# Kernel tuning notes

Measured on AMD Instinct MI355X. Metric: run time of the kernel, lower is better.

The kernel has to match this reference:

```python
import jax, jax.numpy as jnp
import numpy as np

B, N, F_IN, T = 4, 512, 64, 16
K, F_CHEB, F_TIME, TS = 3, 64, 64, 1
E = 16384
LN_EPS = 1e-5


def setup_inputs() -> dict:
    key = jax.random.key(0)
    ks = jax.random.split(key, 18)
    s = 0.05
    X = jax.random.normal(ks[0], (B, N, F_IN, T), jnp.float32)
    # edges with guaranteed no self-loops (so remove_self_loops is a no-op)
    src = jax.random.randint(ks[1], (E,), 0, N, jnp.int32)
    off = jax.random.randint(ks[2], (E,), 1, N, jnp.int32)
    dst = (src + off) % N
    edge_index = jnp.stack([src, dst])
    return {
        'X': X,
        'edge_index': edge_index,
        'U1': jax.random.uniform(ks[3], (N,)) * s,
        'U2': jax.random.normal(ks[4], (F_IN, N)) * s,
        'U3': jax.random.uniform(ks[5], (F_IN,)) * s,
        'be': jax.random.normal(ks[6], (1, T, T)) * s,
        'Ve': jax.random.normal(ks[7], (T, T)) * s,
        'Ws1': jax.random.uniform(ks[8], (T,)) * s,
        'Ws2': jax.random.normal(ks[9], (F_IN, T)) * s,
        'Ws3': jax.random.uniform(ks[10], (F_IN,)) * s,
        'bs': jax.random.normal(ks[11], (1, N, N)) * s,
        'Vs': jax.random.normal(ks[12], (N, N)) * s,
        'W_cheb': jax.random.normal(ks[13], (K, F_IN, F_CHEB)) * s,
        'b_cheb': jax.random.uniform(ks[14], (F_CHEB,)) * s,
        'Wt': jax.random.normal(ks[15], (F_TIME, F_CHEB, 1, 3)) * s,
        'bt': jnp.zeros((F_TIME,), jnp.float32),
        'Wr': jax.random.normal(ks[16], (F_TIME, F_IN, 1, 1)) * s,
        'br': jnp.zeros((F_TIME,), jnp.float32),
        'gamma': jnp.ones((F_TIME,), jnp.float32),
        'beta': jnp.zeros((F_TIME,), jnp.float32),
    }


def _forward(edge_index, X, U1, U2, U3, be, Ve, Ws1, Ws2, Ws3, bs, Vs,
             W_cheb, b_cheb, Wt, bt, Wr, br, gamma, beta):
    Bn, Nn, Fn, Tn = X.shape
    # ---- temporal attention: (B,T,T)
    lhs_t = jnp.einsum('bnft,n->btf', X, U1) @ U2            # (B,T,N)
    rhs_t = jnp.einsum('f,bnft->bnt', U3, X)                 # (B,N,T)
    Et = jnp.matmul(Ve, jax.nn.sigmoid(jnp.matmul(lhs_t, rhs_t) + be))
    Et = jax.nn.softmax(Et, axis=1)
    # temporally re-weighted signal
    Xt = jnp.matmul(X.reshape(Bn, Nn * Fn, Tn), Et).reshape(Bn, Nn, Fn, Tn)
    # ---- spatial attention: (B,N,N)
    lhs_s = jnp.einsum('bnft,t->bnf', Xt, Ws1) @ Ws2         # (B,N,T)
    rhs_s = jnp.einsum('f,bnft->btn', Ws3, Xt)               # (B,T,N)
    S = jnp.matmul(Vs, jax.nn.sigmoid(jnp.matmul(lhs_s, rhs_s) + bs))
    S = jax.nn.softmax(S, axis=1)                            # (B,N,N)
    # ---- scaled sym-normalized Laplacian; lambda_max=2 so 2/lambda_max = 1.
    # edges: -D^-1/2 A D^-1/2 (E), +I self loops (N), then add_self_loops(-1) (N)
    row, col = edge_index[0], edge_index[1]
    ew = jnp.ones(row.shape, X.dtype)
    deg = jnp.zeros((Nn,), X.dtype).at[row].add(ew)
    dis = jnp.where(deg > 0, 1.0 / jnp.sqrt(jnp.maximum(deg, 1.0)), 0.0)  # deg is integral so max() only guards deg==0
    wn = -dis[row] * dis[col]
    loops = jnp.arange(Nn)
    rows = jnp.concatenate([row, loops, loops])
    cols = jnp.concatenate([col, loops, loops])
    norm = jnp.concatenate([wn, jnp.ones((Nn,), X.dtype), -jnp.ones((Nn,), X.dtype)])
    att_norm = norm[None, :] * S[:, rows, cols]              # (B,Etot)

    def prop(h, w):
        # propagate over transposed edges: gather at col, scatter-add at row
        # h: (B,T,N,F); w broadcastable to (B,1,Etot)
        msg = w[..., None] * h[:, :, cols, :]
        return jnp.zeros_like(h).at[:, :, rows, :].add(msg)

    xt = X.transpose(0, 3, 1, 2)                             # (B,T,N,F): ChebConv applied per timestep
    Tx0 = jnp.diagonal(S, axis1=1, axis2=2)[:, None, :, None] * xt  # diag(S) @ x
    out = jnp.einsum('btnf,fg->btng', Tx0, W_cheb[0])
    if W_cheb.shape[0] > 1:
        Tx1 = prop(Tx0, att_norm[:, None, :])
        out = out + jnp.einsum('btnf,fg->btng', Tx1, W_cheb[1])
    for k in range(2, W_cheb.shape[0]):
        Tx2 = 2.0 * prop(Tx1, norm[None, None, :]) - Tx0
        out = out + jnp.einsum('btnf,fg->btng', Tx2, W_cheb[k])
        Tx0, Tx1 = Tx1, Tx2
    X_hat = jax.nn.relu(out + b_cheb)                        # (B,T,N,Fc)
    # ---- time conv (1x3, stride (1,TS)) on (B,Fc,N,T) + residual 1x1 conv
    conv_t = jax.lax.conv_general_dilated(
        X_hat.transpose(0, 3, 2, 1), Wt, (1, TS), ((0, 0), (1, 1)),
        dimension_numbers=('NCHW', 'OIHW', 'NCHW')) + bt[None, :, None, None]
    conv_r = jax.lax.conv_general_dilated(
        X.transpose(0, 2, 1, 3), Wr, (1, TS), ((0, 0), (0, 0)),
        dimension_numbers=('NCHW', 'OIHW', 'NCHW')) + br[None, :, None, None]
    Z = jax.nn.relu(conv_r + conv_t).transpose(0, 3, 2, 1)   # (B,T,N,Ft)
    mu = jnp.mean(Z, -1, keepdims=True)
    var = jnp.var(Z, -1, keepdims=True)
    Z = (Z - mu) / jnp.sqrt(var + LN_EPS) * gamma + beta     # LayerNorm over Ft
    return Z.transpose(0, 2, 3, 1)                           # (B,N,Ft,T)


def reference(X, edge_index, U1, U2, U3, be, Ve, Ws1, Ws2, Ws3, bs, Vs,
              W_cheb, b_cheb, Wt, bt, Wr, br, gamma, beta):
    return _forward(edge_index, X, U1, U2, U3, be, Ve, Ws1, Ws2, Ws3, bs, Vs,
                    W_cheb, b_cheb, Wt, bt, Wr, br, gamma, beta)
```

## Files before the change

### kernel.cpp

```cpp
#include <hip/hip_runtime.h>
#include <math.h>

#define NB 4
#define NV 512
#define NF 64
#define NT 16
#define NE 16384

#define TX1_OFF    2097152u
#define SIGT_OFF   4194304u
#define ST_OFF     TX1_OFF
#define BST_OFF    8388608u
#define ET_OFF     8650752u
#define PART_OFF   8651776u
#define RHST_OFF   8684544u
#define LHSS_OFF   8717312u
#define RHSSN_OFF  8750080u
#define DIAGS_OFF  8782848u
#define CSRW_OFF   8850432u
#define WTT_OFF    8866816u
#define WRT_OFF    8879104u
#define RHS3_OFF   8883712u
#define EW1_OFF    8916480u
#define MPART_OFF  8916544u
#define FEND       8949312u

__global__ void k_prep(const int* __restrict__ ei, int* __restrict__ counts,
                       const float* __restrict__ Wt, const float* __restrict__ Wr,
                       const float* __restrict__ bs,
                       float* __restrict__ WtT, float* __restrict__ WrT,
                       float* __restrict__ bsT,
                       const float* __restrict__ X, const float* __restrict__ U1,
                       const float* __restrict__ U3, const float* __restrict__ Ws3,
                       float* __restrict__ part, float* __restrict__ rhs,
                       float* __restrict__ rhs3) {
    __shared__ int h[512];
    __shared__ float tile[64][65];
    int bid = blockIdx.x, tid = threadIdx.x;
    if (bid < 64) {
        int c = bid;
        h[tid] = 0; h[tid + 256] = 0;
        __syncthreads();
        atomicAdd(&h[ei[c * 256 + tid]], 1);
        __syncthreads();
        counts[c * 512 + tid] = h[tid];
        counts[c * 512 + tid + 256] = h[tid + 256];
    } else if (bid < 128) {
        int tb = bid - 64;
        int r0 = (tb >> 3) * 64, c0 = (tb & 7) * 64;
        int c = tid & 63, rq = tid >> 6;
        for (int k = 0; k < 16; ++k) {
            int r = rq * 16 + k;
            tile[r][c] = bs[(r0 + r) * 512 + c0 + c];
        }
        __syncthreads();
        int r2 = tid & 63;
        for (int k = 0; k < 16; ++k) {
            int c2 = rq * 16 + k;
            bsT[(size_t)(c0 + c2) * 512 + r0 + r2] = tile[r2][c2];
        }
    } else if (bid < 192) {
        int idx = (bid - 128) * 256 + tid;
        if (idx < 12288) {
            int o = idx & 63, gd = idx >> 6;
            int g = gd / 3, dt = gd - g * 3;
            WtT[idx] = Wt[(o * 64 + g) * 3 + dt];
        } else {
            int i2 = idx - 12288;
            int o = i2 & 63, f = i2 >> 6;
            WrT[i2] = Wr[o * 64 + f];
        }
    } else {
        int sub = bid - 192;
        if (sub < 32) {
            int b = sub >> 3, g = sub & 7;
            float acc[4] = {0.f, 0.f, 0.f, 0.f};
            const float* Xb = X + (size_t)b * NV * 1024;
            int n0 = g * 64;
            for (int nn = 0; nn < 64; ++nn) {
                int n = n0 + nn;
                float u = U1[n];
                const float* xp = Xb + (size_t)n * 1024;
#pragma unroll
                for (int k = 0; k < 4; ++k) acc[k] += xp[tid + 256 * k] * u;
            }
#pragma unroll
            for (int k = 0; k < 4; ++k) part[(size_t)(b * 8 + g) * 1024 + tid + 256 * k] = acc[k];
        } else {
            int gid = (sub - 32) * 256 + tid;
            int t = gid & 15;
            const float* xp = X + ((size_t)(gid >> 4)) * 1024 + t;
            float a = 0.f, a3 = 0.f;
#pragma unroll
            for (int f = 0; f < 64; ++f) {
                float v = xp[f * 16];
                a += U3[f] * v;
                a3 += Ws3[f] * v;
            }
            rhs[gid] = a;
            rhs3[gid] = a3;
        }
    }
}

__global__ __launch_bounds__(512) void k_graph(const int* __restrict__ ei,
                                               const int* __restrict__ counts,
                                               int* __restrict__ row_start,
                                               int* __restrict__ csr_col,
                                               float* __restrict__ csr_w,
                                               const float* __restrict__ rhs_g,
                                               const float* __restrict__ U2,
                                               float* __restrict__ Mpart) {
    __shared__ int sc[512];
    __shared__ int base_l[512];
    __shared__ float dis_l[512];
    __shared__ int rs_l[512];
    __shared__ int rowL[256];
    __shared__ float rhsL[1024];
    int bid = blockIdx.x, tid = threadIdx.x;
    if (bid < 64) {
        int c = bid;
        int r = tid;
        int sum = 0, base = 0;
        for (int cc = 0; cc < 64; ++cc) {
            if (cc == c) base = sum;
            sum += counts[cc * 512 + r];
        }
        base_l[r] = base;
        dis_l[r] = sum > 0 ? 1.0f / sqrtf((float)sum) : 0.0f;
        sc[r] = sum;
        __syncthreads();
        for (int off = 1; off < 512; off <<= 1) {
            int v = sc[r];
            int add = (r >= off) ? sc[r - off] : 0;
            __syncthreads();
            sc[r] = v + add;
            __syncthreads();
        }
        rs_l[r] = sc[r] - sum;
        if (c == 0) {
            row_start[r] = sc[r] - sum;
            if (r == 511) row_start[512] = sc[r];
        }
        if (tid < 256) rowL[tid] = ei[c * 256 + tid];
        __syncthreads();
        if (tid < 256) {
            int rr = rowL[tid];
            int col = ei[NE + c * 256 + tid];
            int rank = 0;
            for (int j = 0; j < tid; ++j)
                if (rowL[j] == rr) rank++;
            int pos = rs_l[rr] + base_l[rr] + rank;
            csr_col[pos] = col;
            csr_w[pos] = -dis_l[rr] * dis_l[col];
        }
    } else {
        int sub = bid - 64;
        int b = sub >> 3, g = sub & 7;
        rhsL[tid] = rhs_g[(size_t)b * 8192 + g * 1024 + tid];
        rhsL[tid + 512] = rhs_g[(size_t)b * 8192 + g * 1024 + tid + 512];
        __syncthreads();
        float acc[2] = {0.f, 0.f};
        int fA[2], tA[2];
#pragma unroll
        for (int k = 0; k < 2; ++k) { int idx = tid + 512 * k; fA[k] = idx >> 4; tA[k] = idx & 15; }
        int n0 = g * 64;
        for (int nn = 0; nn < 64; ++nn) {
#pragma unroll
            for (int k = 0; k < 2; ++k)
                acc[k] += U2[fA[k] * 512 + n0 + nn] * rhsL[nn * 16 + tA[k]];
        }
#pragma unroll
        for (int k = 0; k < 2; ++k) Mpart[(size_t)(b * 8 + g) * 1024 + tid + 512 * k] = acc[k];
    }
}

__global__ void k_temporal(const float* __restrict__ part, const float* __restrict__ Mpart,
                           const float* __restrict__ be,
                           const float* __restrict__ Ve, const float* __restrict__ Ws1,
                           float* __restrict__ Et, float* __restrict__ ew1) {
    __shared__ float lhs1[1024];
    __shared__ float M[1024];
    __shared__ float Esig[256];
    __shared__ float Et0[256];
    __shared__ float red[32];
    __shared__ float EtL[256];
    int b = blockIdx.x, tid = threadIdx.x;
#pragma unroll
    for (int k = 0; k < 4; ++k) {
        int idx = tid + 256 * k;
        float s = 0.f, m = 0.f;
        for (int g = 0; g < 8; ++g) {
            s += part[(size_t)(b * 8 + g) * 1024 + idx];
            m += Mpart[(size_t)(b * 8 + g) * 1024 + idx];
        }
        lhs1[idx] = s;
        M[idx] = m;
    }
    __syncthreads();
    {
        int t1 = tid >> 4, t2 = tid & 15;
        float s = 0.f;
        for (int f = 0; f < 64; ++f) s += lhs1[f * 16 + t1] * M[f * 16 + t2];
        s += be[t1 * 16 + t2];
        Esig[tid] = 1.f / (1.f + expf(-s));
    }
    __syncthreads();
    {
        int t1 = tid >> 4, t2 = tid & 15;
        float s = 0.f;
        for (int k = 0; k < 16; ++k) s += Ve[t1 * 16 + k] * Esig[k * 16 + t2];
        Et0[tid] = s;
    }
    __syncthreads();
    if (tid < 16) {
        float m = -1e30f;
        for (int k = 0; k < 16; ++k) m = fmaxf(m, Et0[k * 16 + tid]);
        float s = 0.f;
        for (int k = 0; k < 16; ++k) s += expf(Et0[k * 16 + tid] - m);
        red[tid] = m; red[16 + tid] = 1.f / s;
    }
    __syncthreads();
    {
        int t2 = tid & 15;
        float etv = expf(Et0[tid] - red[t2]) * red[16 + t2];
        Et[b * 256 + tid] = etv;
        EtL[tid] = etv;
    }
    __syncthreads();
    if (tid < 16) {
        float s = 0.f;
        for (int t = 0; t < 16; ++t) s += EtL[tid * 16 + t] * Ws1[t];
        ew1[b * 16 + tid] = s;
    }
}

__global__ __launch_bounds__(256) void k_spat2(const float* __restrict__ X,
                                               const float* __restrict__ ew1,
                                               const float* __restrict__ rhs3,
                                               const float* __restrict__ Et,
                                               const float* __restrict__ Ws2,
                                               float* __restrict__ lhs_s,
                                               float* __restrict__ rhs_sn) {
    int wv = threadIdx.x >> 6, lane = threadIdx.x & 63;
    int bn = blockIdx.x * 4 + wv;
    int b = bn >> 9;
    const float4* xp = (const float4*)(X + (size_t)bn * 1024 + lane * 16);
    float4 x0 = xp[0], x1 = xp[1], x2 = xp[2], x3 = xp[3];
    const float* e1 = ew1 + b * 16;
    float l1 = x0.x * e1[0] + x0.y * e1[1] + x0.z * e1[2] + x0.w * e1[3]
             + x1.x * e1[4] + x1.y * e1[5] + x1.z * e1[6] + x1.w * e1[7]
             + x2.x * e1[8] + x2.y * e1[9] + x2.z * e1[10] + x2.w * e1[11]
             + x3.x * e1[12] + x3.y * e1[13] + x3.z * e1[14] + x3.w * e1[15];
    const float4* wp = (const float4*)(Ws2 + lane * 16);
    float4 w0 = wp[0], w1 = wp[1], w2 = wp[2], w3 = wp[3];
    float p[16] = {l1 * w0.x, l1 * w0.y, l1 * w0.z, l1 * w0.w,
                   l1 * w1.x, l1 * w1.y, l1 * w1.z, l1 * w1.w,
                   l1 * w2.x, l1 * w2.y, l1 * w2.z, l1 * w2.w,
                   l1 * w3.x, l1 * w3.y, l1 * w3.z, l1 * w3.w};
#pragma unroll
    for (int off = 32; off; off >>= 1) {
#pragma unroll
        for (int k = 0; k < 16; ++k) p[k] += __shfl_xor(p[k], off);
    }
    if (lane == 0) {
        float4* lp = (float4*)(lhs_s + (size_t)bn * 16);
        lp[0] = make_float4(p[0], p[1], p[2], p[3]);
        lp[1] = make_float4(p[4], p[5], p[6], p[7]);
        lp[2] = make_float4(p[8], p[9], p[10], p[11]);
        lp[3] = make_float4(p[12], p[13], p[14], p[15]);
    }
    if (lane < 16) {
        const float* r3 = rhs3 + (size_t)bn * 16;
        const float* Eb = Et + b * 256;
        float s = 0.f;
#pragma unroll
        for (int tp = 0; tp < 16; ++tp) s += r3[tp] * Eb[tp * 16 + lane];
        rhs_sn[(size_t)bn * 16 + lane] = s;
    }
}

__global__ void k_sigT(const float* __restrict__ lhs_s, const float* __restrict__ rhs_sn,
                       const float* __restrict__ bsT, float* __restrict__ sigT) {
    int gid = blockIdx.x * 256 + threadIdx.x;
    int k = gid & 511, j = (gid >> 9) & 511, b = gid >> 18;
    const float4* lp = (const float4*)(lhs_s + (size_t)(b * 512 + k) * 16);
    const float4* rp = (const float4*)(rhs_sn + (size_t)(b * 512 + j) * 16);
    float s = 0.f;
#pragma unroll
    for (int q = 0; q < 4; ++q) {
        float4 a = lp[q], c = rp[q];
        s += a.x * c.x + a.y * c.y + a.z * c.z + a.w * c.w;
    }
    s += bsT[(size_t)j * 512 + k];
    sigT[gid] = 1.f / (1.f + expf(-s));
}

__global__ __launch_bounds__(256) void k_gemm_s(const float* __restrict__ sigT,
                                                const float* __restrict__ Vs,
                                                float* __restrict__ S0T) {
    __shared__ float As[32 * 68];
    __shared__ float Bs[32 * 68];
    int bI = blockIdx.x, bJ = blockIdx.y, b = blockIdx.z;
    int tid = threadIdx.x, tx = tid & 15, ty = tid >> 4;
    float acc[4][4] = {};
    const float* Ab = sigT + ((size_t)b * 512 + bJ * 64) * 512;
    const float* Bb = Vs + (size_t)bI * 64 * 512;
    for (int k0 = 0; k0 < 512; k0 += 32) {
#pragma unroll
        for (int p = 0; p < 2; ++p) {
            int idx = tid + 256 * p;
            int row = idx >> 3, kk = (idx & 7) * 4;
            float4 a = *(const float4*)(Ab + (size_t)row * 512 + k0 + kk);
            As[(kk + 0) * 68 + row] = a.x; As[(kk + 1) * 68 + row] = a.y;
            As[(kk + 2) * 68 + row] = a.z; As[(kk + 3) * 68 + row] = a.w;
            float4 v = *(const float4*)(Bb + (size_t)row * 512 + k0 + kk);
            Bs[(kk + 0) * 68 + row] = v.x; Bs[(kk + 1) * 68 + row] = v.y;
            Bs[(kk + 2) * 68 + row] = v.z; Bs[(kk + 3) * 68 + row] = v.w;
        }
        __syncthreads();
#pragma unroll
        for (int kk = 0; kk < 32; ++kk) {
            float4 a = *(const float4*)(As + kk * 68 + ty * 4);
            float4 bv = *(const float4*)(Bs + kk * 68 + tx * 4);
            acc[0][0] += a.x * bv.x; acc[0][1] += a.x * bv.y; acc[0][2] += a.x * bv.z; acc[0][3] += a.x * bv.w;
            acc[1][0] += a.y * bv.x; acc[1][1] += a.y * bv.y; acc[1][2] += a.y * bv.z; acc[1][3] += a.y * bv.w;
            acc[2][0] += a.z * bv.x; acc[2][1] += a.z * bv.y; acc[2][2] += a.z * bv.z; acc[2][3] += a.z * bv.w;
            acc[3][0] += a.w * bv.x; acc[3][1] += a.w * bv.y; acc[3][2] += a.w * bv.z; acc[3][3] += a.w * bv.w;
        }
        __syncthreads();
    }
    float* Cb = S0T + ((size_t)b * 512 + bJ * 64) * 512 + bI * 64;
#pragma unroll
    for (int y = 0; y < 4; ++y) {
        int j = ty * 4 + y;
        *(float4*)(Cb + (size_t)j * 512 + tx * 4) =
            make_float4(acc[y][0], acc[y][1], acc[y][2], acc[y][3]);
    }
}

__global__ void k_softmax_s(float* __restrict__ ST, float* __restrict__ diagS) {
    __shared__ float red[4];
    int bj = blockIdx.x;
    int b = bj >> 9, j = bj & 511;
    float* row = ST + (size_t)bj * 512;
    int tid = threadIdx.x;
    float v0 = row[tid], v1 = row[tid + 256];
    float m = fmaxf(v0, v1);
    for (int off = 32; off; off >>= 1) m = fmaxf(m, __shfl_xor(m, off));
    if ((tid & 63) == 0) red[tid >> 6] = m;
    __syncthreads();
    m = fmaxf(fmaxf(red[0], red[1]), fmaxf(red[2], red[3]));
    __syncthreads();
    float e0 = expf(v0 - m), e1 = expf(v1 - m);
    float s = e0 + e1;
    for (int off = 32; off; off >>= 1) s += __shfl_xor(s, off);
    if ((tid & 63) == 0) red[tid >> 6] = s;
    __syncthreads();
    s = red[0] + red[1] + red[2] + red[3];
    float inv = 1.f / s;
    float r0 = e0 * inv, r1 = e1 * inv;
    row[tid] = r0;
    row[tid + 256] = r1;
    if (j < 256) { if (tid == j) diagS[b * 512 + j] = r0; }
    else { if (tid == j - 256) diagS[b * 512 + j] = r1; }
}

__global__ __launch_bounds__(256) void k_prop1(const float* __restrict__ X,
                                               const float* __restrict__ ST,
                                               const float* __restrict__ diagS,
                                               const float* __restrict__ csr_w,
                                               const int* __restrict__ csr_col,
                                               const int* __restrict__ row_start,
                                               float* __restrict__ Tx1) {
    int blk = ((blockIdx.x & 7) << 8) + (blockIdx.x >> 3);
    int b = blk >> 9, i = blk & 511;
    int tid = threadIdx.x;
    int s = row_start[i], e2 = row_start[i + 1];
    const float4* Xb = (const float4*)(X + (size_t)b * 512 * 1024);
    const float* STb = ST + (size_t)b * 512 * 512;
    const float* dSb = diagS + b * 512;
    float4 acc = make_float4(0.f, 0.f, 0.f, 0.f);
    for (int p = s; p < e2; ++p) {
        int col = csr_col[p];
        float w = csr_w[p] * STb[(size_t)col * 512 + i] * dSb[col];
        float4 v = Xb[col * 256 + tid];
        acc.x += w * v.x; acc.y += w * v.y; acc.z += w * v.z; acc.w += w * v.w;
    }
    *(float4*)(Tx1 + (size_t)blk * 1024 + tid * 4) = acc;
}

__global__ __launch_bounds__(256) void k_pco(const float* __restrict__ X,
                                             const float* __restrict__ Tx1,
                                             const float* __restrict__ diagS,
                                             const float* __restrict__ csr_w,
                                             const int* __restrict__ csr_col,
                                             const int* __restrict__ row_start,
                                             const float* __restrict__ Wc,
                                             const float* __restrict__ bc,
                                             const float* __restrict__ WtT,
                                             const float* __restrict__ WrT,
                                             const float* __restrict__ bt,
                                             const float* __restrict__ br,
                                             const float* __restrict__ gamma,
                                             const float* __restrict__ beta,
                                             float* __restrict__ out) {
    __shared__ float buf[4160];
    __shared__ float xl[1024];
    __shared__ float xh[1280];
    int blk = ((blockIdx.x & 7) << 8) + (blockIdx.x >> 3);
    int b = blk >> 9, i = blk & 511;
    int tid = threadIdx.x;
#pragma unroll
    for (int k = 0; k < 5; ++k) xh[tid + 256 * k] = 0.f;
    int s = row_start[i], e2 = row_start[i + 1];
    const float* T1b = Tx1 + (size_t)b * 512 * 1024 + tid * 4;
    float4 acc = make_float4(0.f, 0.f, 0.f, 0.f);
    for (int p = s; p < e2; ++p) {
        int col = csr_col[p];
        float w = csr_w[p];
        float4 v = *(const float4*)(T1b + (size_t)col * 1024);
        acc.x += w * v.x; acc.y += w * v.y; acc.z += w * v.z; acc.w += w * v.w;
    }
    float ds = diagS[blk];
    size_t roff = (size_t)blk * 1024 + tid * 4;
    float4 x0 = *(const float4*)(X + roff);
    float4 t1v = *(const float4*)(Tx1 + roff);
    float4 t0v, t2v;
    t2v.x = 2.f * acc.x - ds * x0.x;
    t2v.y = 2.f * acc.y - ds * x0.y;
    t2v.z = 2.f * acc.z - ds * x0.z;
    t2v.w = 2.f * acc.w - ds * x0.w;
    t0v.x = x0.x * ds; t0v.y = x0.y * ds; t0v.z = x0.z * ds; t0v.w = x0.w * ds;
    *(float4*)(buf + tid * 4) = t0v;
    *(float4*)(buf + 1024 + tid * 4) = t1v;
    *(float4*)(buf + 2048 + tid * 4) = t2v;
    *(float4*)(xl + tid * 4) = x0;
    __syncthreads();
    {
        int g = tid >> 2, t4 = (tid & 3) * 4;
        float bcg = bc[g];
        float4 accg = make_float4(bcg, bcg, bcg, bcg);
        const float* t0s = buf;
        const float* t1s = buf + 1024;
        const float* t2s = buf + 2048;
        for (int f = 0; f < 64; ++f) {
            float w0 = Wc[f * 64 + g];
            float w1 = Wc[4096 + f * 64 + g];
            float w2 = Wc[8192 + f * 64 + g];
            float4 a0 = *(const float4*)(t0s + f * 16 + t4);
            float4 a1 = *(const float4*)(t1s + f * 16 + t4);
            float4 a2 = *(const float4*)(t2s + f * 16 + t4);
            accg.x += w0 * a0.x + w1 * a1.x + w2 * a2.x;
            accg.y += w0 * a0.y + w1 * a1.y + w2 * a2.y;
            accg.z += w0 * a0.z + w1 * a1.z + w2 * a2.z;
            accg.w += w0 * a0.w + w1 * a1.w + w2 * a2.w;
        }
        xh[g * 20 + t4 + 1] = fmaxf(accg.x, 0.f);
        xh[g * 20 + t4 + 2] = fmaxf(accg.y, 0.f);
        xh[g * 20 + t4 + 3] = fmaxf(accg.z, 0.f);
        xh[g * 20 + t4 + 4] = fmaxf(accg.w, 0.f);
    }
    __syncthreads();
    float* red = buf;
    int o = tid & 63, q = tid >> 6;
    float accv[16];
#pragma unroll
    for (int k = 0; k < 16; ++k) accv[k] = 0.f;
    for (int gi = 0; gi < 16; ++gi) {
        int g = q * 16 + gi;
        const float4* xp = (const float4*)(xh + g * 20);
        float4 xa = xp[0], xb = xp[1], xc = xp[2], xd = xp[3], xe = xp[4];
        float xs[20] = {xa.x, xa.y, xa.z, xa.w, xb.x, xb.y, xb.z, xb.w,
                        xc.x, xc.y, xc.z, xc.w, xd.x, xd.y, xd.z, xd.w,
                        xe.x, xe.y, xe.z, xe.w};
        float w0 = WtT[(g * 3 + 0) * 64 + o];
        float w1 = WtT[(g * 3 + 1) * 64 + o];
        float w2 = WtT[(g * 3 + 2) * 64 + o];
#pragma unroll
        for (int tt = 0; tt < 16; ++tt)
            accv[tt] += xs[tt] * w0 + xs[tt + 1] * w1 + xs[tt + 2] * w2;
    }
    for (int fi = 0; fi < 16; ++fi) {
        int f = q * 16 + fi;
        const float4* xp = (const float4*)(xl + f * 16);
        float4 xa = xp[0], xb = xp[1], xc = xp[2], xd = xp[3];
        float xs[16] = {xa.x, xa.y, xa.z, xa.w, xb.x, xb.y, xb.z, xb.w,
                        xc.x, xc.y, xc.z, xc.w, xd.x, xd.y, xd.z, xd.w};
        float w = WrT[f * 64 + o];
#pragma unroll
        for (int tt = 0; tt < 16; ++tt) accv[tt] += xs[tt] * w;
    }
#pragma unroll
    for (int tt = 0; tt < 16; ++tt) red[q * 1024 + tt * 64 + o] = accv[tt];
    __syncthreads();
    float bsum = bt[o] + br[o];
    float go = gamma[o], bo = beta[o];
    float zv4[4];
#pragma unroll
    for (int tt = 0; tt < 4; ++tt) {
        int t = q * 4 + tt;
        float sv = bsum;
#pragma unroll
        for (int qq = 0; qq < 4; ++qq) sv += red[qq * 1024 + t * 64 + o];
        zv4[tt] = fmaxf(sv, 0.f);
    }
    __syncthreads();
#pragma unroll
    for (int tt = 0; tt < 4; ++tt) {
        int t = q * 4 + tt;
        float zv = zv4[tt];
        float sv = zv, sq = zv * zv;
        for (int off = 32; off; off >>= 1) {
            sv += __shfl_xor(sv, off);
            sq += __shfl_xor(sq, off);
        }
        float mu = sv * (1.f / 64.f);
        float var = sq * (1.f / 64.f) - mu * mu;
        red[t * 65 + o] = (zv - mu) * rsqrtf(var + 1e-5f) * go + bo;
    }
    __syncthreads();
#pragma unroll
    for (int k = 0; k < 4; ++k) {
        int idx = tid + 256 * k;
        out[(size_t)blk * 1024 + idx] = red[(idx & 15) * 65 + (idx >> 4)];
    }
}

extern "C" void kernel_launch(void* const* d_in, const int* in_sizes, int n_in,
                              void* d_out, int out_size, void* d_ws, size_t ws_size,
                              hipStream_t stream) {
    const float* X     = (const float*)d_in[0];
    const int*   ei    = (const int*)d_in[1];
    const float* U1    = (const float*)d_in[2];
    const float* U2    = (const float*)d_in[3];
    const float* U3    = (const float*)d_in[4];
    const float* be    = (const float*)d_in[5];
    const float* Ve    = (const float*)d_in[6];
    const float* Ws1   = (const float*)d_in[7];
    const float* Ws2   = (const float*)d_in[8];
    const float* Ws3   = (const float*)d_in[9];
    const float* bs    = (const float*)d_in[10];
    const float* Vs    = (const float*)d_in[11];
    const float* Wc    = (const float*)d_in[12];
    const float* bc    = (const float*)d_in[13];
    const float* Wt    = (const float*)d_in[14];
    const float* bt    = (const float*)d_in[15];
    const float* Wr    = (const float*)d_in[16];
    const float* br    = (const float*)d_in[17];
    const float* gamma = (const float*)d_in[18];
    const float* beta  = (const float*)d_in[19];

    float* ws = (float*)d_ws;
    float* Tx1    = ws + TX1_OFF;
    float* ST     = ws + ST_OFF;
    float* sigT   = ws + SIGT_OFF;
    float* bsT    = ws + BST_OFF;
    float* Et     = ws + ET_OFF;
    float* part   = ws + PART_OFF;
    float* rhs_t  = ws + RHST_OFF;
    float* lhs_s  = ws + LHSS_OFF;
    float* rhs_sn = ws + RHSSN_OFF;
    float* diagS  = ws + DIAGS_OFF;
    float* csr_w  = ws + CSRW_OFF;
    float* WtT    = ws + WTT_OFF;
    float* WrT    = ws + WRT_OFF;
    float* rhs3   = ws + RHS3_OFF;
    float* ew1    = ws + EW1_OFF;
    float* Mpart  = ws + MPART_OFF;

    int* ib        = (int*)(ws + FEND);
    int* row_start = ib;
    int* csr_col   = ib + 516;
    int* counts    = csr_col + NE;

    k_prep<<<352, 256, 0, stream>>>(ei, counts, Wt, Wr, bs, WtT, WrT, bsT,
                                    X, U1, U3, Ws3, part, rhs_t, rhs3);
    k_graph<<<96, 512, 0, stream>>>(ei, counts, row_start, csr_col, csr_w,
                                    rhs_t, U2, Mpart);

    k_temporal<<<4, 256, 0, stream>>>(part, Mpart, be, Ve, Ws1, Et, ew1);

    k_spat2<<<512, 256, 0, stream>>>(X, ew1, rhs3, Et, Ws2, lhs_s, rhs_sn);
    k_sigT<<<4096, 256, 0, stream>>>(lhs_s, rhs_sn, bsT, sigT);
    k_gemm_s<<<dim3(8, 8, 4), 256, 0, stream>>>(sigT, Vs, ST);
    k_softmax_s<<<2048, 256, 0, stream>>>(ST, diagS);

    k_prop1<<<2048, 256, 0, stream>>>(X, ST, diagS, csr_w, csr_col, row_start, Tx1);
    k_pco<<<2048, 256, 0, stream>>>(X, Tx1, diagS, csr_w, csr_col, row_start,
                                    Wc, bc, WtT, WrT, bt, br, gamma, beta,
                                    (float*)d_out);
}
```

Baseline: 146.7 us.

## Transpose Cheb weights, fold T0 scaling, and split time-conv work by time groups

Adds a transposed copy of the Chebyshev weights in the prep kernel so each thread in k_pco reads its weights as contiguous float4. The T0 term is now formed on the fly from the shared X tile times diagS, which drops one shared buffer. The time conv and residual conv are restructured so each thread computes all 64 input channels for 4 time steps, instead of 16 time steps over a quarter of the channels. This removes the cross-quarter shared-memory reduction and one barrier, at the cost of longer per-thread loops with more weight loads.

```diff
diff --git a/kernel.cpp b/kernel.cpp
--- a/kernel.cpp
+++ b/kernel.cpp
@@ -23,13 +23,14 @@
 #define RHS3_OFF   8883712u
 #define EW1_OFF    8916480u
 #define MPART_OFF  8916544u
-#define FEND       8949312u
+#define WCT_OFF    8949312u
+#define FEND       8961600u
 
 __global__ void k_prep(const int* __restrict__ ei, int* __restrict__ counts,
                        const float* __restrict__ Wt, const float* __restrict__ Wr,
-                       const float* __restrict__ bs,
+                       const float* __restrict__ Wc, const float* __restrict__ bs,
                        float* __restrict__ WtT, float* __restrict__ WrT,
-                       float* __restrict__ bsT,
+                       float* __restrict__ WcT, float* __restrict__ bsT,
                        const float* __restrict__ X, const float* __restrict__ U1,
                        const float* __restrict__ U3, const float* __restrict__ Ws3,
                        float* __restrict__ part, float* __restrict__ rhs,
@@ -70,8 +71,13 @@
             int o = i2 & 63, f = i2 >> 6;
             WrT[i2] = Wr[o * 64 + f];
         }
+    } else if (bid < 240) {
+        int idx = (bid - 192) * 256 + tid;
+        int g = idx / 192, rem = idx - g * 192;
+        int k = rem >> 6, f = rem & 63;
+        WcT[idx] = Wc[k * 4096 + f * 64 + g];
     } else {
-        int sub = bid - 192;
+        int sub = bid - 240;
         if (sub < 32) {
             int b = sub >> 3, g = sub & 7;
             float acc[4] = {0.f, 0.f, 0.f, 0.f};
@@ -396,7 +402,7 @@
                                              const float* __restrict__ csr_w,
                                              const int* __restrict__ csr_col,
                                              const int* __restrict__ row_start,
-                                             const float* __restrict__ Wc,
+                                             const float* __restrict__ WcT,
                                              const float* __restrict__ bc,
                                              const float* __restrict__ WtT,
                                              const float* __restrict__ WrT,
@@ -405,7 +411,7 @@
                                              const float* __restrict__ gamma,
                                              const float* __restrict__ beta,
                                              float* __restrict__ out) {
-    __shared__ float buf[4160];
+    __shared__ float buf[2048];
     __shared__ float xl[1024];
     __shared__ float xh[1280];
     int blk = ((blockIdx.x & 7) << 8) + (blockIdx.x >> 3);
@@ -426,35 +432,41 @@
     size_t roff = (size_t)blk * 1024 + tid * 4;
     float4 x0 = *(const float4*)(X + roff);
     float4 t1v = *(const float4*)(Tx1 + roff);
-    float4 t0v, t2v;
+    float4 t2v;
     t2v.x = 2.f * acc.x - ds * x0.x;
     t2v.y = 2.f * acc.y - ds * x0.y;
     t2v.z = 2.f * acc.z - ds * x0.z;
     t2v.w = 2.f * acc.w - ds * x0.w;
-    t0v.x = x0.x * ds; t0v.y = x0.y * ds; t0v.z = x0.z * ds; t0v.w = x0.w * ds;
-    *(float4*)(buf + tid * 4) = t0v;
-    *(float4*)(buf + 1024 + tid * 4) = t1v;
-    *(float4*)(buf + 2048 + tid * 4) = t2v;
+    *(float4*)(buf + tid * 4) = t1v;
+    *(float4*)(buf + 1024 + tid * 4) = t2v;
     *(float4*)(xl + tid * 4) = x0;
     __syncthreads();
     {
         int g = tid >> 2, t4 = (tid & 3) * 4;
         float bcg = bc[g];
         float4 accg = make_float4(bcg, bcg, bcg, bcg);
-        const float* t0s = buf;
-        const float* t1s = buf + 1024;
-        const float* t2s = buf + 2048;
-        for (int f = 0; f < 64; ++f) {
-            float w0 = Wc[f * 64 + g];
-            float w1 = Wc[4096 + f * 64 + g];
-            float w2 = Wc[8192 + f * 64 + g];
-            float4 a0 = *(const float4*)(t0s + f * 16 + t4);
-            float4 a1 = *(const float4*)(t1s + f * 16 + t4);
-            float4 a2 = *(const float4*)(t2s + f * 16 + t4);
-            accg.x += w0 * a0.x + w1 * a1.x + w2 * a2.x;
-            accg.y += w0 * a0.y + w1 * a1.y + w2 * a2.y;
-            accg.z += w0 * a0.z + w1 * a1.z + w2 * a2.z;
-            accg.w += w0 * a0.w + w1 * a1.w + w2 * a2.w;
+        const float* t1s = buf;
+        const float* t2s = buf + 1024;
+        const float* wgp = WcT + g * 192;
+        for (int f0 = 0; f0 < 64; f0 += 4) {
+            float4 wq0 = *(const float4*)(wgp + f0);
+            float4 wq1 = *(const float4*)(wgp + 64 + f0);
+            float4 wq2 = *(const float4*)(wgp + 128 + f0);
+#pragma unroll
+            for (int ff = 0; ff < 4; ++ff) {
+                int f = f0 + ff;
+                float w0 = ff == 0 ? wq0.x : ff == 1 ? wq0.y : ff == 2 ? wq0.z : wq0.w;
+                float w1 = ff == 0 ? wq1.x : ff == 1 ? wq1.y : ff == 2 ? wq1.z : wq1.w;
+                float w2 = ff == 0 ? wq2.x : ff == 1 ? wq2.y : ff == 2 ? wq2.z : wq2.w;
+                float4 xv = *(const float4*)(xl + f * 16 + t4);
+                float4 a1 = *(const float4*)(t1s + f * 16 + t4);
+                float4 a2 = *(const float4*)(t2s + f * 16 + t4);
+                float a0x = ds * xv.x, a0y = ds * xv.y, a0z = ds * xv.z, a0w = ds * xv.w;
+                accg.x += w0 * a0x + w1 * a1.x + w2 * a2.x;
+                accg.y += w0 * a0y + w1 * a1.y + w2 * a2.y;
+                accg.z += w0 * a0z + w1 * a1.z + w2 * a2.z;
+                accg.w += w0 * a0w + w1 * a1.w + w2 * a2.w;
+            }
         }
         xh[g * 20 + t4 + 1] = fmaxf(accg.x, 0.f);
         xh[g * 20 + t4 + 2] = fmaxf(accg.y, 0.f);
@@ -462,54 +474,30 @@
         xh[g * 20 + t4 + 4] = fmaxf(accg.w, 0.f);
     }
     __syncthreads();
-    float* red = buf;
-    int o = tid & 63, q = tid >> 6;
-    float accv[16];
-#pragma unroll
-    for (int k = 0; k < 16; ++k) accv[k] = 0.f;
-    for (int gi = 0; gi < 16; ++gi) {
-        int g = q * 16 + gi;
-        const float4* xp = (const float4*)(xh + g * 20);
-        float4 xa = xp[0], xb = xp[1], xc = xp[2], xd = xp[3], xe = xp[4];
-        float xs[20] = {xa.x, xa.y, xa.z, xa.w, xb.x, xb.y, xb.z, xb.w,
-                        xc.x, xc.y, xc.z, xc.w, xd.x, xd.y, xd.z, xd.w,
-                        xe.x, xe.y, xe.z, xe.w};
+    float* z = buf;
+    int o = tid & 63, tg = tid >> 6;
+    float accv[4] = {0.f, 0.f, 0.f, 0.f};
+    for (int g = 0; g < 64; ++g) {
         float w0 = WtT[(g * 3 + 0) * 64 + o];
         float w1 = WtT[(g * 3 + 1) * 64 + o];
         float w2 = WtT[(g * 3 + 2) * 64 + o];
-#pragma unroll
-        for (int tt = 0; tt < 16; ++tt)
-            accv[tt] += xs[tt] * w0 + xs[tt + 1] * w1 + xs[tt + 2] * w2;
-    }
-    for (int fi = 0; fi < 16; ++fi) {
-        int f = q * 16 + fi;
-        const float4* xp = (const float4*)(xl + f * 16);
-        float4 xa = xp[0], xb = xp[1], xc = xp[2], xd = xp[3];
-        float xs[16] = {xa.x, xa.y, xa.z, xa.w, xb.x, xb.y, xb.z, xb.w,
-                        xc.x, xc.y, xc.z, xc.w, xd.x, xd.y, xd.z, xd.w};
+        const float* xg = xh + g * 20 + tg * 4;
+#pragma unroll
+        for (int tt = 0; tt < 4; ++tt)
+            accv[tt] += xg[tt] * w0 + xg[tt + 1] * w1 + xg[tt + 2] * w2;
+    }
+    for (int f = 0; f < 64; ++f) {
         float w = WrT[f * 64 + o];
-#pragma unroll
-        for (int tt = 0; tt < 16; ++tt) accv[tt] += xs[tt] * w;
-    }
-#pragma unroll
-    for (int tt = 0; tt < 16; ++tt) red[q * 1024 + tt * 64 + o] = accv[tt];
-    __syncthreads();
+        const float* xf = xl + f * 16 + tg * 4;
+#pragma unroll
+        for (int tt = 0; tt < 4; ++tt) accv[tt] += xf[tt] * w;
+    }
     float bsum = bt[o] + br[o];
     float go = gamma[o], bo = beta[o];
-    float zv4[4];
 #pragma unroll
     for (int tt = 0; tt < 4; ++tt) {
-        int t = q * 4 + tt;
-        float sv = bsum;
-#pragma unroll
-        for (int qq = 0; qq < 4; ++qq) sv += red[qq * 1024 + t * 64 + o];
-        zv4[tt] = fmaxf(sv, 0.f);
-    }
-    __syncthreads();
-#pragma unroll
-    for (int tt = 0; tt < 4; ++tt) {
-        int t = q * 4 + tt;
-        float zv = zv4[tt];
+        int t = tg * 4 + tt;
+        float zv = fmaxf(bsum + accv[tt], 0.f);
         float sv = zv, sq = zv * zv;
         for (int off = 32; off; off >>= 1) {
             sv += __shfl_xor(sv, off);
@@ -517,13 +505,13 @@
         }
         float mu = sv * (1.f / 64.f);
         float var = sq * (1.f / 64.f) - mu * mu;
-        red[t * 65 + o] = (zv - mu) * rsqrtf(var + 1e-5f) * go + bo;
+        z[t * 65 + o] = (zv - mu) * rsqrtf(var + 1e-5f) * go + bo;
     }
     __syncthreads();
 #pragma unroll
     for (int k = 0; k < 4; ++k) {
         int idx = tid + 256 * k;
-        out[(size_t)blk * 1024 + idx] = red[(idx & 15) * 65 + (idx >> 4)];
+        out[(size_t)blk * 1024 + idx] = z[(idx & 15) * 65 + (idx >> 4)];
     }
 }
 
@@ -568,13 +556,14 @@
     float* rhs3   = ws + RHS3_OFF;
     float* ew1    = ws + EW1_OFF;
     float* Mpart  = ws + MPART_OFF;
+    float* WcT    = ws + WCT_OFF;
 
     int* ib        = (int*)(ws + FEND);
     int* row_start = ib;
     int* csr_col   = ib + 516;
     int* counts    = csr_col + NE;
 
-    k_prep<<<352, 256, 0, stream>>>(ei, counts, Wt, Wr, bs, WtT, WrT, bsT,
+    k_prep<<<400, 256, 0, stream>>>(ei, counts, Wt, Wr, Wc, bs, WtT, WrT, WcT, bsT,
                                     X, U1, U3, Ws3, part, rhs_t, rhs3);
     k_graph<<<96, 512, 0, stream>>>(ei, counts, row_start, csr_col, csr_w,
                                     rhs_t, U2, Mpart);
@@ -588,6 +577,6 @@
 
     k_prop1<<<2048, 256, 0, stream>>>(X, ST, diagS, csr_w, csr_col, row_start, Tx1);
     k_pco<<<2048, 256, 0, stream>>>(X, Tx1, diagS, csr_w, csr_col, row_start,
-                                    Wc, bc, WtT, WrT, bt, br, gamma, beta,
+                                    WcT, bc, WtT, WrT, bt, br, gamma, beta,
                                     (float*)d_out);
 }
```

New measurement: 157.7 us. 1.07x slower.
